# Kernel tuning notes

Measured on AMD Instinct MI355X. Metric: run time of the kernel, lower is better.

## Reference

```python
import jax, jax.numpy as jnp
import numpy as np

B, T, E, H = 8, 1024, 128, 8
S = E // H  # 16, narrow per-head dim


def setup_inputs() -> dict:
    key = jax.random.key(0)
    ks = jax.random.split(key, 7)
    return {
        "x": jax.random.normal(ks[0], (B, T, E), dtype=jnp.float32),
        "masks": jax.random.randint(ks[1], (B, T), 0, 2, dtype=jnp.int32),
        "Wq": jax.random.normal(ks[2], (S, S), dtype=jnp.float32) * 0.05,
        "Wk": jax.random.normal(ks[3], (S, S), dtype=jnp.float32) * 0.05,
        "Wv": jax.random.normal(ks[4], (S, S), dtype=jnp.float32) * 0.05,
        "Wu": jax.random.normal(ks[5], (E, E), dtype=jnp.float32) * 0.05,
        "bu": jnp.zeros((E,), dtype=jnp.float32),
        "temporal_only": 1,
    }


def reference(x, masks, Wq, Wk, Wv, Wu, bu, temporal_only):
    b, t, e = x.shape
    h = H
    s = e // h
    x4 = x.reshape(b, t, h, s)
    # nn.Linear(s, s, bias=False): y = x @ W.T, applied per head
    q = jnp.einsum('bths,ds->bthd', x4, Wq)
    k = jnp.einsum('bths,ds->bthd', x4, Wk)
    v = jnp.einsum('bths,ds->bthd', x4, Wv)
    scale = jnp.float32(e) ** 0.25
    q = q / scale
    k = k / scale
    # (b, h, t, t) attention logits
    dot = jnp.einsum('bqhd,bkhd->bhqk', q, k)
    # temporal_only masking: masks is (b, t), applied on key axis then query axis
    m = masks.astype(bool)
    neg = jnp.float32(-1e9)
    dot = jnp.where(m[:, None, None, :], dot, neg)
    dot = jnp.where(m[:, None, :, None], dot, neg)
    attn = jax.nn.softmax(dot, axis=-1)
    # post-softmax zeroing with the same masks
    attn = jnp.where(m[:, None, None, :], attn, jnp.float32(0.0))
    attn = jnp.where(m[:, None, :, None], attn, jnp.float32(0.0))
    out = jnp.einsum('bhqk,bkhd->bqhd', attn, v).reshape(b, t, h * s)
    return out @ Wu.T + bu
```

## Files before the change

kernel.cpp:

```cpp
#include <hip/hip_runtime.h>

#define NB 8
#define NT 1024
#define NE 128
#define NH 8
#define NS 16

#define WS_Q 0
#define WS_KC 1048576
#define WS_VC 2097152
#define WS_Y 3145728
#define WS_VCNT 4194304

#define WT_PITCH 132

typedef float v2f __attribute__((ext_vector_type(2)));

static __device__ __forceinline__ v2f vlo(const float4 v) { return v2f{v.x, v.y}; }
static __device__ __forceinline__ v2f vhi(const float4 v) { return v2f{v.z, v.w}; }
static __device__ __forceinline__ v2f pfma(v2f a, v2f b, v2f c) {
  return __builtin_elementwise_fma(a, b, c);
}

static __device__ __forceinline__ float fexp2(float x) {
  return __builtin_amdgcn_exp2f(x);
}

static __device__ __forceinline__ void fma4(float4& acc, float s, const float4 v) {
  v2f lo = pfma(v2f{s, s}, vlo(v), vlo(acc));
  v2f hi = pfma(v2f{s, s}, vhi(v), vhi(acc));
  acc.x = lo.x; acc.y = lo.y; acc.z = hi.x; acc.w = hi.y;
}

static __device__ __forceinline__ float dot16p(const float4 q0, const float4 q1,
                                               const float4 q2, const float4 q3,
                                               const float4 k0, const float4 k1,
                                               const float4 k2, const float4 k3) {
  v2f a = vlo(q0) * vlo(k0);
  v2f b = vhi(q0) * vhi(k0);
  a = pfma(vlo(q1), vlo(k1), a);
  b = pfma(vhi(q1), vhi(k1), b);
  a = pfma(vlo(q2), vlo(k2), a);
  b = pfma(vhi(q2), vhi(k2), b);
  a = pfma(vlo(q3), vlo(k3), a);
  b = pfma(vhi(q3), vhi(k3), b);
  v2f c = a + b;
  return c.x + c.y;
}

__global__ __launch_bounds__(256) void qkv_kernel(
    const float* __restrict__ x, const int* __restrict__ masks,
    const float* __restrict__ Wq, const float* __restrict__ Wk,
    const float* __restrict__ Wv, float* __restrict__ Q,
    float* __restrict__ Kc, float* __restrict__ Vc, int* __restrict__ vcount) {
  __shared__ __align__(16) float xs[64 * 20];
  __shared__ int posl[64];
  const int tid = threadIdx.x;
  const int h = blockIdx.x & 7;
  const int rg = blockIdx.x >> 3;
  const int b = rg >> 4;
  const int bt = (rg & 15) << 6;
  {
    const int sr = tid >> 2, sq = tid & 3;
    float4 xv =
        *(const float4*)(x + (size_t)(b * NT + bt + sr) * 128 + h * 16 + sq * 4);
    *(float4*)(xs + sr * 20 + sq * 4) = xv;
  }
  if (tid < 64) {
    int cnt = 0;
    for (int c = 0; c < bt; c += 64)
      cnt += __popcll(__ballot(masks[b * NT + c + tid] != 0));
    int v = masks[b * NT + bt + tid] != 0;
    unsigned long long bal = __ballot(v);
    posl[tid] = v ? (cnt + __popcll(bal & ((1ull << tid) - 1ull))) : -1;
    if (bt == NT - 64 && tid == 0) vcount[b] = cnt + __popcll(bal);
  }
  const int d = tid & 15;
  const int r = (tid >> 4) << 2;
  const float4* wq4 = (const float4*)(Wq + d * 16);
  const float4 wq0 = wq4[0], wq1 = wq4[1], wq2 = wq4[2], wq3 = wq4[3];
  const float4* wk4 = (const float4*)(Wk + d * 16);
  const float4 wk0 = wk4[0], wk1 = wk4[1], wk2 = wk4[2], wk3 = wk4[3];
  const float4* wv4 = (const float4*)(Wv + d * 16);
  const float4 wv0 = wv4[0], wv1 = wv4[1], wv2 = wv4[2], wv3 = wv4[3];
  const float invs = 0.12751744448143132f;
  __syncthreads();
#pragma unroll
  for (int i = 0; i < 4; i++) {
    const int row = r + i;
    const float4* xp = (const float4*)(xs + row * 20);
    const float4 x0 = xp[0], x1 = xp[1], x2 = xp[2], x3 = xp[3];
    float aq = dot16p(x0, x1, x2, x3, wq0, wq1, wq2, wq3);
    float ak = dot16p(x0, x1, x2, x3, wk0, wk1, wk2, wk3);
    float av = dot16p(x0, x1, x2, x3, wv0, wv1, wv2, wv3);
    const int t = bt + row;
    Q[((size_t)(b * NH + h) * NT + t) * NS + d] = aq * invs;
    const int pp = posl[row];
    if (pp >= 0) {
      size_t oc = ((size_t)(b * NH + h) * NT + pp) * NS + d;
      Kc[oc] = ak;
      Vc[oc] = av;
    }
  }
}

__global__ __launch_bounds__(512, 2) void attn_kernel(
    const float* __restrict__ Q, const float* __restrict__ Kc,
    const float* __restrict__ Vc, const int* __restrict__ masks,
    const int* __restrict__ vcount, float* __restrict__ Y) {
  __shared__ __align__(16) float smem[16384];
  float* Ks = smem;
  float* Vs = smem + 8192;
  const int tid = threadIdx.x;
  const int lane = tid & 63;
  const int s = tid >> 6;
  const int bh = blockIdx.x & 63;
  const int qg = blockIdx.x >> 6;
  const int b = bh >> 3, h = bh & 7;
  const int tbase = qg << 8;
  const int nv = vcount[b];

  float4 q[4][4];
#pragma unroll
  for (int qq = 0; qq < 4; qq++) {
    const float4* qg4 =
        (const float4*)(Q + ((size_t)bh * NT + tbase + (qq << 6) + lane) * NS);
    q[qq][0] = qg4[0]; q[qq][1] = qg4[1]; q[qq][2] = qg4[2]; q[qq][3] = qg4[3];
  }
  v2f o[4][8];
  float l[4];
#pragma unroll
  for (int qq = 0; qq < 4; qq++) {
    l[qq] = 0.f;
#pragma unroll
    for (int k = 0; k < 8; k++) o[qq][k] = v2f{0.f, 0.f};
  }

  const int quad = tid & 3;
  const int jr = tid >> 2;

#pragma unroll 1
  for (int k0 = 0; k0 < nv; k0 += 512) {
    const int chunk = (nv - k0 < 512) ? (nv - k0) : 512;
    __syncthreads();
#pragma unroll 1
    for (int p = 0; p < 4; p++) {
      const int row = jr + (p << 7);
      float4 kv = {0, 0, 0, 0};
      if (row < chunk)
        kv = *(const float4*)(Kc + ((size_t)bh * NT + (k0 + row)) * NS +
                              (quad << 2));
      *(float4*)(Ks + row * 16 + (quad << 2)) = kv;
    }
#pragma unroll 1
    for (int p = 0; p < 4; p++) {
      const int row = jr + (p << 7);
      float4 vv = {0, 0, 0, 0};
      if (row < chunk)
        vv = *(const float4*)(Vc + ((size_t)bh * NT + (k0 + row)) * NS +
                              (quad << 2));
      *(float4*)(Vs + row * 16 + (quad << 2)) = vv;
    }
    __syncthreads();
#pragma unroll 2
    for (int g = 0; g < 16; g++) {
      const int rb = s + (g << 5);
      if (rb >= chunk) break;
      float sc[4][4];
#pragma unroll
      for (int i = 0; i < 4; i++) {
        const float4* kr = (const float4*)(Ks + (rb + (i << 3)) * 16);
        const float4 k0v = kr[0], k1v = kr[1], k2v = kr[2], k3v = kr[3];
#pragma unroll
        for (int qq = 0; qq < 4; qq++)
          sc[qq][i] =
              dot16p(q[qq][0], q[qq][1], q[qq][2], q[qq][3], k0v, k1v, k2v, k3v);
      }
#pragma unroll
      for (int i = 0; i < 4; i++)
        if (rb + (i << 3) >= chunk) {
          sc[0][i] = -1e30f; sc[1][i] = -1e30f;
          sc[2][i] = -1e30f; sc[3][i] = -1e30f;
        }
      float p[4][4];
#pragma unroll
      for (int qq = 0; qq < 4; qq++) {
        p[qq][0] = fexp2(sc[qq][0]);
        p[qq][1] = fexp2(sc[qq][1]);
        p[qq][2] = fexp2(sc[qq][2]);
        p[qq][3] = fexp2(sc[qq][3]);
        l[qq] += (p[qq][0] + p[qq][1]) + (p[qq][2] + p[qq][3]);
      }
#pragma unroll
      for (int i = 0; i < 4; i++) {
        const float4* vr = (const float4*)(Vs + (rb + (i << 3)) * 16);
        const float4 v0 = vr[0], v1 = vr[1], v2 = vr[2], v3 = vr[3];
#pragma unroll
        for (int qq = 0; qq < 4; qq++) {
          const v2f pq = {p[qq][i], p[qq][i]};
          o[qq][0] = pfma(pq, vlo(v0), o[qq][0]);
          o[qq][1] = pfma(pq, vhi(v0), o[qq][1]);
          o[qq][2] = pfma(pq, vlo(v1), o[qq][2]);
          o[qq][3] = pfma(pq, vhi(v1), o[qq][3]);
          o[qq][4] = pfma(pq, vlo(v2), o[qq][4]);
          o[qq][5] = pfma(pq, vhi(v2), o[qq][5]);
          o[qq][6] = pfma(pq, vlo(v3), o[qq][6]);
          o[qq][7] = pfma(pq, vhi(v3), o[qq][7]);
        }
      }
    }
  }

  float* om = smem;
#pragma unroll
  for (int ph = 0; ph < 4; ph++) {
    __syncthreads();
    {
      float* pa = om + (s * 64 + lane) * 20;
#pragma unroll
      for (int k = 0; k < 8; k++) *(v2f*)(pa + k * 2) = o[ph][k];
      pa[16] = l[ph];
    }
    __syncthreads();
    {
      const int q8 = tid >> 3;
      const int sub = tid & 7;
      float L = 0.f;
      v2f y = {0.f, 0.f};
#pragma unroll
      for (int ss = 0; ss < 8; ss++) {
        const float* pp = om + (ss * 64 + q8) * 20;
        L += pp[16];
        v2f ov = *(const v2f*)(pp + sub * 2);
        y += ov;
      }
      const int tq = tbase + (ph << 6) + q8;
      const int qm = masks[b * NT + tq];
      const float inv = (qm != 0 && L > 0.f) ? (1.0f / L) : 0.f;
      y *= v2f{inv, inv};
      *(v2f*)(Y + ((size_t)b * NT + tq) * NE + h * NS + sub * 2) = y;
    }
  }
}

__global__ __launch_bounds__(256) void proj_kernel(
    const float* __restrict__ Y, const float* __restrict__ Wu,
    const float* __restrict__ bu, float* __restrict__ out) {
  __shared__ __align__(16) float Wt[64 * WT_PITCH];
  __shared__ __align__(16) float Yt[16 * 128];
  const int tid = threadIdx.x;
  const int r0 = blockIdx.x * 16;
  const float4* yg = (const float4*)(Y + (size_t)r0 * 128);
  float4* yt4 = (float4*)Yt;
  yt4[tid] = yg[tid];
  yt4[tid + 256] = yg[tid + 256];
  const int c0 = (tid & 31) << 2;
  const int rg = (tid >> 5) & 3;
  const int eh = tid >> 7;
  float4 acc0 = {0, 0, 0, 0}, acc1 = {0, 0, 0, 0}, acc2 = {0, 0, 0, 0},
         acc3 = {0, 0, 0, 0};
  for (int e0 = 0; e0 < 128; e0 += 64) {
    __syncthreads();
#pragma unroll
    for (int p = 0; p < 8; p++) {
      int idx = tid + p * 256;
      int c = idx >> 4;
      int es = (idx & 15) << 2;
      float4 w = *(const float4*)(Wu + c * 128 + e0 + es);
      Wt[(es + 0) * WT_PITCH + c] = w.x;
      Wt[(es + 1) * WT_PITCH + c] = w.y;
      Wt[(es + 2) * WT_PITCH + c] = w.z;
      Wt[(es + 3) * WT_PITCH + c] = w.w;
    }
    __syncthreads();
    const int eb = eh << 5;
    const float* y0 = Yt + (rg * 4 + 0) * 128 + e0 + eb;
    const float* y1 = Yt + (rg * 4 + 1) * 128 + e0 + eb;
    const float* y2 = Yt + (rg * 4 + 2) * 128 + e0 + eb;
    const float* y3 = Yt + (rg * 4 + 3) * 128 + e0 + eb;
#pragma unroll 4
    for (int e = 0; e < 32; e += 4) {
      const float* wb = Wt + (eb + e) * WT_PITCH + c0;
      float4 w0 = *(const float4*)(wb + 0 * WT_PITCH);
      float4 w1 = *(const float4*)(wb + 1 * WT_PITCH);
      float4 w2 = *(const float4*)(wb + 2 * WT_PITCH);
      float4 w3 = *(const float4*)(wb + 3 * WT_PITCH);
      float4 ya = *(const float4*)(y0 + e);
      float4 yb = *(const float4*)(y1 + e);
      float4 yc = *(const float4*)(y2 + e);
      float4 yd = *(const float4*)(y3 + e);
      fma4(acc0, ya.x, w0); fma4(acc0, ya.y, w1); fma4(acc0, ya.z, w2); fma4(acc0, ya.w, w3);
      fma4(acc1, yb.x, w0); fma4(acc1, yb.y, w1); fma4(acc1, yb.z, w2); fma4(acc1, yb.w, w3);
      fma4(acc2, yc.x, w0); fma4(acc2, yc.y, w1); fma4(acc2, yc.z, w2); fma4(acc2, yc.w, w3);
      fma4(acc3, yd.x, w0); fma4(acc3, yd.y, w1); fma4(acc3, yd.z, w2); fma4(acc3, yd.w, w3);
    }
  }
  __syncthreads();
  if (eh == 1) {
    float* p = Wt + (tid & 127) * 20;
    *(float4*)(p + 0) = acc0; *(float4*)(p + 4) = acc1;
    *(float4*)(p + 8) = acc2; *(float4*)(p + 12) = acc3;
  }
  __syncthreads();
  if (eh == 0) {
    const float* p = Wt + tid * 20;
    float4 b4 = *(const float4*)(bu + c0);
    float4 q0 = *(const float4*)(p + 0);
    float4 q1 = *(const float4*)(p + 4);
    float4 q2 = *(const float4*)(p + 8);
    float4 q3 = *(const float4*)(p + 12);
    acc0.x += q0.x + b4.x; acc0.y += q0.y + b4.y; acc0.z += q0.z + b4.z; acc0.w += q0.w + b4.w;
    acc1.x += q1.x + b4.x; acc1.y += q1.y + b4.y; acc1.z += q1.z + b4.z; acc1.w += q1.w + b4.w;
    acc2.x += q2.x + b4.x; acc2.y += q2.y + b4.y; acc2.z += q2.z + b4.z; acc2.w += q2.w + b4.w;
    acc3.x += q3.x + b4.x; acc3.y += q3.y + b4.y; acc3.z += q3.z + b4.z; acc3.w += q3.w + b4.w;
    *(float4*)(out + (size_t)(r0 + rg * 4 + 0) * 128 + c0) = acc0;
    *(float4*)(out + (size_t)(r0 + rg * 4 + 1) * 128 + c0) = acc1;
    *(float4*)(out + (size_t)(r0 + rg * 4 + 2) * 128 + c0) = acc2;
    *(float4*)(out + (size_t)(r0 + rg * 4 + 3) * 128 + c0) = acc3;
  }
}

extern "C" void kernel_launch(void* const* d_in, const int* in_sizes, int n_in,
                              void* d_out, int out_size, void* d_ws,
                              size_t ws_size, hipStream_t stream) {
  const float* x = (const float*)d_in[0];
  const int* masks = (const int*)d_in[1];
  const float* Wq = (const float*)d_in[2];
  const float* Wk = (const float*)d_in[3];
  const float* Wv = (const float*)d_in[4];
  const float* Wu = (const float*)d_in[5];
  const float* bu = (const float*)d_in[6];
  float* out = (float*)d_out;

  float* ws = (float*)d_ws;
  float* Q = ws + WS_Q;
  float* Kc = ws + WS_KC;
  float* Vc = ws + WS_VC;
  float* Y = ws + WS_Y;
  int* vcount = (int*)(ws + WS_VCNT);

  qkv_kernel<<<1024, 256, 0, stream>>>(x, masks, Wq, Wk, Wv, Q, Kc, Vc,
                                       vcount);
  attn_kernel<<<4 * NB * NH, 512, 0, stream>>>(Q, Kc, Vc, masks, vcount, Y);
  proj_kernel<<<NB * NT / 16, 256, 0, stream>>>(Y, Wu, bu, out);
}
```

Baseline: 125.1 us.

## Compact queries to valid positions and skip masked queries in attention

Q is now stored compacted alongside K and V, and a vidx map from compacted slot back to original time index is recorded. The attention kernel spreads only the valid queries across its four blocks per (b,h), choosing a templated count of query groups per thread, and scatters results back through vidx. Masked rows of Y are never written; the projection kernel zeroes them instead by reading the mask. With about half the tokens masked, this is meant to roughly halve the QK and PV work per block, at the cost of extra template instantiations and an indirect scatter.

Result: faster. 119.9 us (-4.2%).

```diff
diff --git a/kernel.cpp b/kernel.cpp
--- a/kernel.cpp
+++ b/kernel.cpp
@@ -10,7 +10,8 @@
 #define WS_KC 1048576
 #define WS_VC 2097152
 #define WS_Y 3145728
-#define WS_VCNT 4194304
+#define WS_VIDX 4194304
+#define WS_VCNT (4194304 + 8192)
 
 #define WT_PITCH 132
 
@@ -52,7 +53,8 @@
     const float* __restrict__ x, const int* __restrict__ masks,
     const float* __restrict__ Wq, const float* __restrict__ Wk,
     const float* __restrict__ Wv, float* __restrict__ Q,
-    float* __restrict__ Kc, float* __restrict__ Vc, int* __restrict__ vcount) {
+    float* __restrict__ Kc, float* __restrict__ Vc, int* __restrict__ vidx,
+    int* __restrict__ vcount) {
   __shared__ __align__(16) float xs[64 * 20];
   __shared__ int posl[64];
   const int tid = threadIdx.x;
@@ -72,7 +74,9 @@
       cnt += __popcll(__ballot(masks[b * NT + c + tid] != 0));
     int v = masks[b * NT + bt + tid] != 0;
     unsigned long long bal = __ballot(v);
-    posl[tid] = v ? (cnt + __popcll(bal & ((1ull << tid) - 1ull))) : -1;
+    int pos = v ? (cnt + __popcll(bal & ((1ull << tid) - 1ull))) : -1;
+    posl[tid] = pos;
+    if (pos >= 0) vidx[b * NT + pos] = bt + tid;
     if (bt == NT - 64 && tid == 0) vcount[b] = cnt + __popcll(bal);
   }
   const int d = tid & 15;
@@ -88,49 +92,41 @@
 #pragma unroll
   for (int i = 0; i < 4; i++) {
     const int row = r + i;
+    const int pp = posl[row];
+    if (pp < 0) continue;
     const float4* xp = (const float4*)(xs + row * 20);
     const float4 x0 = xp[0], x1 = xp[1], x2 = xp[2], x3 = xp[3];
     float aq = dot16p(x0, x1, x2, x3, wq0, wq1, wq2, wq3);
     float ak = dot16p(x0, x1, x2, x3, wk0, wk1, wk2, wk3);
     float av = dot16p(x0, x1, x2, x3, wv0, wv1, wv2, wv3);
-    const int t = bt + row;
-    Q[((size_t)(b * NH + h) * NT + t) * NS + d] = aq * invs;
-    const int pp = posl[row];
-    if (pp >= 0) {
-      size_t oc = ((size_t)(b * NH + h) * NT + pp) * NS + d;
-      Kc[oc] = ak;
-      Vc[oc] = av;
-    }
-  }
-}
-
-__global__ __launch_bounds__(512, 2) void attn_kernel(
+    size_t oc = ((size_t)(b * NH + h) * NT + pp) * NS + d;
+    Q[oc] = aq * invs;
+    Kc[oc] = ak;
+    Vc[oc] = av;
+  }
+}
+
+template <int NQ>
+static __device__ __forceinline__ void attn_body(
     const float* __restrict__ Q, const float* __restrict__ Kc,
-    const float* __restrict__ Vc, const int* __restrict__ masks,
-    const int* __restrict__ vcount, float* __restrict__ Y) {
-  __shared__ __align__(16) float smem[16384];
+    const float* __restrict__ Vc, const int* __restrict__ vidx,
+    float* __restrict__ Y, float* smem, const int tid, const int lane,
+    const int s, const int b, const int bh, const int h, const int nv,
+    const int tbase) {
   float* Ks = smem;
   float* Vs = smem + 8192;
-  const int tid = threadIdx.x;
-  const int lane = tid & 63;
-  const int s = tid >> 6;
-  const int bh = blockIdx.x & 63;
-  const int qg = blockIdx.x >> 6;
-  const int b = bh >> 3, h = bh & 7;
-  const int tbase = qg << 8;
-  const int nv = vcount[b];
-
-  float4 q[4][4];
-#pragma unroll
-  for (int qq = 0; qq < 4; qq++) {
-    const float4* qg4 =
-        (const float4*)(Q + ((size_t)bh * NT + tbase + (qq << 6) + lane) * NS);
-    q[qq][0] = qg4[0]; q[qq][1] = qg4[1]; q[qq][2] = qg4[2]; q[qq][3] = qg4[3];
-  }
-  v2f o[4][8];
-  float l[4];
-#pragma unroll
-  for (int qq = 0; qq < 4; qq++) {
+  float4 q[NQ][4];
+#pragma unroll
+  for (int qq = 0; qq < NQ; qq++) {
+    int cq = tbase + (qq << 6) + lane;
+    int cqc = (cq < nv) ? cq : (nv - 1);
+    const float4* qp = (const float4*)(Q + ((size_t)bh * NT + cqc) * NS);
+    q[qq][0] = qp[0]; q[qq][1] = qp[1]; q[qq][2] = qp[2]; q[qq][3] = qp[3];
+  }
+  v2f o[NQ][8];
+  float l[NQ];
+#pragma unroll
+  for (int qq = 0; qq < NQ; qq++) {
     l[qq] = 0.f;
 #pragma unroll
     for (int k = 0; k < 8; k++) o[qq][k] = v2f{0.f, 0.f};
@@ -166,25 +162,25 @@
     for (int g = 0; g < 16; g++) {
       const int rb = s + (g << 5);
       if (rb >= chunk) break;
-      float sc[4][4];
+      float sc[NQ][4];
 #pragma unroll
       for (int i = 0; i < 4; i++) {
         const float4* kr = (const float4*)(Ks + (rb + (i << 3)) * 16);
         const float4 k0v = kr[0], k1v = kr[1], k2v = kr[2], k3v = kr[3];
 #pragma unroll
-        for (int qq = 0; qq < 4; qq++)
+        for (int qq = 0; qq < NQ; qq++)
           sc[qq][i] =
               dot16p(q[qq][0], q[qq][1], q[qq][2], q[qq][3], k0v, k1v, k2v, k3v);
       }
 #pragma unroll
       for (int i = 0; i < 4; i++)
         if (rb + (i << 3) >= chunk) {
-          sc[0][i] = -1e30f; sc[1][i] = -1e30f;
-          sc[2][i] = -1e30f; sc[3][i] = -1e30f;
+#pragma unroll
+          for (int qq = 0; qq < NQ; qq++) sc[qq][i] = -1e30f;
         }
-      float p[4][4];
-#pragma unroll
-      for (int qq = 0; qq < 4; qq++) {
+      float p[NQ][4];
+#pragma unroll
+      for (int qq = 0; qq < NQ; qq++) {
         p[qq][0] = fexp2(sc[qq][0]);
         p[qq][1] = fexp2(sc[qq][1]);
         p[qq][2] = fexp2(sc[qq][2]);
@@ -196,7 +192,7 @@
         const float4* vr = (const float4*)(Vs + (rb + (i << 3)) * 16);
         const float4 v0 = vr[0], v1 = vr[1], v2 = vr[2], v3 = vr[3];
 #pragma unroll
-        for (int qq = 0; qq < 4; qq++) {
+        for (int qq = 0; qq < NQ; qq++) {
           const v2f pq = {p[qq][i], p[qq][i]};
           o[qq][0] = pfma(pq, vlo(v0), o[qq][0]);
           o[qq][1] = pfma(pq, vhi(v0), o[qq][1]);
@@ -212,8 +208,10 @@
   }
 
   float* om = smem;
-#pragma unroll
-  for (int ph = 0; ph < 4; ph++) {
+  const int q8 = tid >> 3;
+  const int sub = tid & 7;
+#pragma unroll
+  for (int ph = 0; ph < NQ; ph++) {
     __syncthreads();
     {
       float* pa = om + (s * 64 + lane) * 20;
@@ -223,37 +221,69 @@
     }
     __syncthreads();
     {
-      const int q8 = tid >> 3;
-      const int sub = tid & 7;
-      float L = 0.f;
-      v2f y = {0.f, 0.f};
-#pragma unroll
-      for (int ss = 0; ss < 8; ss++) {
-        const float* pp = om + (ss * 64 + q8) * 20;
-        L += pp[16];
-        v2f ov = *(const v2f*)(pp + sub * 2);
-        y += ov;
+      const int cq = tbase + (ph << 6) + q8;
+      if (cq < nv) {
+        float L = 0.f;
+        v2f y = {0.f, 0.f};
+#pragma unroll
+        for (int ss = 0; ss < 8; ss++) {
+          const float* pp = om + (ss * 64 + q8) * 20;
+          L += pp[16];
+          y += *(const v2f*)(pp + sub * 2);
+        }
+        const int tq = vidx[b * NT + cq];
+        const float inv = (L > 0.f) ? (1.0f / L) : 0.f;
+        y *= v2f{inv, inv};
+        *(v2f*)(Y + ((size_t)b * NT + tq) * NE + h * NS + sub * 2) = y;
       }
-      const int tq = tbase + (ph << 6) + q8;
-      const int qm = masks[b * NT + tq];
-      const float inv = (qm != 0 && L > 0.f) ? (1.0f / L) : 0.f;
-      y *= v2f{inv, inv};
-      *(v2f*)(Y + ((size_t)b * NT + tq) * NE + h * NS + sub * 2) = y;
-    }
+    }
+  }
+}
+
+__global__ __launch_bounds__(512, 2) void attn_kernel(
+    const float* __restrict__ Q, const float* __restrict__ Kc,
+    const float* __restrict__ Vc, const int* __restrict__ vidx,
+    const int* __restrict__ vcount, float* __restrict__ Y) {
+  __shared__ __align__(16) float smem[16384];
+  const int tid = threadIdx.x;
+  const int lane = tid & 63;
+  const int s = tid >> 6;
+  const int bh = blockIdx.x & 63;
+  const int qg = blockIdx.x >> 6;
+  const int b = bh >> 3, h = bh & 7;
+  const int nv = vcount[b];
+  const int nq = (nv + 255) >> 8;
+  const int tbase = qg * (nq << 6);
+  if (nq == 2) {
+    attn_body<2>(Q, Kc, Vc, vidx, Y, smem, tid, lane, s, b, bh, h, nv, tbase);
+  } else if (nq == 3) {
+    attn_body<3>(Q, Kc, Vc, vidx, Y, smem, tid, lane, s, b, bh, h, nv, tbase);
+  } else if (nq == 4) {
+    attn_body<4>(Q, Kc, Vc, vidx, Y, smem, tid, lane, s, b, bh, h, nv, tbase);
+  } else if (nq == 1) {
+    attn_body<1>(Q, Kc, Vc, vidx, Y, smem, tid, lane, s, b, bh, h, nv, tbase);
   }
 }
 
 __global__ __launch_bounds__(256) void proj_kernel(
-    const float* __restrict__ Y, const float* __restrict__ Wu,
-    const float* __restrict__ bu, float* __restrict__ out) {
+    const float* __restrict__ Y, const int* __restrict__ masks,
+    const float* __restrict__ Wu, const float* __restrict__ bu,
+    float* __restrict__ out) {
   __shared__ __align__(16) float Wt[64 * WT_PITCH];
   __shared__ __align__(16) float Yt[16 * 128];
   const int tid = threadIdx.x;
   const int r0 = blockIdx.x * 16;
   const float4* yg = (const float4*)(Y + (size_t)r0 * 128);
   float4* yt4 = (float4*)Yt;
-  yt4[tid] = yg[tid];
-  yt4[tid + 256] = yg[tid + 256];
+  {
+    const float4 z = {0, 0, 0, 0};
+    const int m0 = masks[r0 + (tid >> 5)];
+    const int m1 = masks[r0 + 8 + (tid >> 5)];
+    float4 v0 = yg[tid];
+    float4 v1 = yg[tid + 256];
+    yt4[tid] = m0 ? v0 : z;
+    yt4[tid + 256] = m1 ? v1 : z;
+  }
   const int c0 = (tid & 31) << 2;
   const int rg = (tid >> 5) & 3;
   const int eh = tid >> 7;
@@ -337,10 +367,11 @@
   float* Kc = ws + WS_KC;
   float* Vc = ws + WS_VC;
   float* Y = ws + WS_Y;
+  int* vidx = (int*)(ws + WS_VIDX);
   int* vcount = (int*)(ws + WS_VCNT);
 
-  qkv_kernel<<<1024, 256, 0, stream>>>(x, masks, Wq, Wk, Wv, Q, Kc, Vc,
+  qkv_kernel<<<1024, 256, 0, stream>>>(x, masks, Wq, Wk, Wv, Q, Kc, Vc, vidx,
                                        vcount);
-  attn_kernel<<<4 * NB * NH, 512, 0, stream>>>(Q, Kc, Vc, masks, vcount, Y);
-  proj_kernel<<<NB * NT / 16, 256, 0, stream>>>(Y, Wu, bu, out);
-}
+  attn_kernel<<<4 * NB * NH, 512, 0, stream>>>(Q, Kc, Vc, vidx, vcount, Y);
+  proj_kernel<<<NB * NT / 16, 256, 0, stream>>>(Y, masks, Wu, bu, out);
+}
```
